# Kernel optimization log

Measured on AMD Instinct MI355X. Metric: run time of the kernel, lower is better.

## Reference

```python
import jax, jax.numpy as jnp
import numpy as np

B, S, E, D, A = 32, 2048, 1024, 1024, 1024


def setup_inputs() -> dict:
    key = jax.random.key(0)
    k1, k2, k3, k4, k5, k6, k7, k8 = jax.random.split(key, 8)
    # Kaiming-uniform-ish init scales (values don't matter for correctness)
    def lin(kw, kb, fan_in, fan_out):
        bound = 1.0 / np.sqrt(fan_in)
        W = jax.random.uniform(kw, (fan_out, fan_in), minval=-bound, maxval=bound, dtype=jnp.float32)
        b = jax.random.uniform(kb, (fan_out,), minval=-bound, maxval=bound, dtype=jnp.float32)
        return W, b
    W_enc, b_enc = lin(k1, k2, E, A)
    W_dec, b_dec = lin(k3, k4, D, A)
    W_v, b_v = lin(k5, k6, A, 1)
    encoder_out = jax.random.normal(k7, (B, S, E), dtype=jnp.float32)
    decoder_hidden = jax.random.normal(k8, (B, D), dtype=jnp.float32)
    return {
        "encoder_out": encoder_out,
        "decoder_hidden": decoder_hidden,
        "W_enc": W_enc, "b_enc": b_enc,
        "W_dec": W_dec, "b_dec": b_dec,
        "W_v": W_v, "b_v": b_v,
    }


def reference(encoder_out, decoder_hidden, W_enc, b_enc, W_dec, b_dec, W_v, b_v):
    # encoder_proj: [B, S, A]
    encoder_proj = jnp.einsum('bse,ae->bsa', encoder_out, W_enc) + b_enc
    # decoder_proj: [B, 1, A]
    decoder_proj = (jnp.einsum('bd,ad->ba', decoder_hidden, W_dec) + b_dec)[:, None, :]
    # scores: [B, S] (V projects attention_dim -> 1)
    scores = jnp.einsum('bsa,a->bs', jnp.tanh(encoder_proj + decoder_proj), W_v[0]) + b_v[0]
    alpha = jax.nn.softmax(scores, axis=1)  # [B, S]
    context = jnp.einsum('bse,bs->be', encoder_out, alpha)  # [B, E]
    return (context, alpha)
```

## Files before the change

kernel.cpp:

```cpp
#include <hip/hip_runtime.h>

typedef unsigned short ushort_t;
typedef __attribute__((ext_vector_type(8))) short short8;
typedef __attribute__((ext_vector_type(4))) float f32x4;


__device__ __forceinline__ ushort_t f2bf(float f) {
    unsigned u = __builtin_bit_cast(unsigned, f);
    u += 0x7fffu + ((u >> 16) & 1u);
    return (ushort_t)(u >> 16);
}

__device__ __forceinline__ float bf2f(ushort_t h) {
    unsigned u = ((unsigned)h) << 16;
    return __builtin_bit_cast(float, u);
}

__device__ __forceinline__ float tanh_fast(float x) {
    float e = __expf(2.0f * x);
    float r = __builtin_amdgcn_rcpf(e + 1.0f);
    return __builtin_fmaf(-2.0f, r, 1.0f);
}

__device__ __forceinline__ void gld16(const ushort_t* g, ushort_t* lds) {
    __builtin_amdgcn_global_load_lds(
        (const __attribute__((address_space(1))) unsigned int*)g,
        (__attribute__((address_space(3))) unsigned int*)lds, 16, 0, 0);
}


__global__ __launch_bounds__(256) void k_front(const float* __restrict__ enc,
                                               const float* __restrict__ Wenc,
                                               const float* __restrict__ dh,
                                               const float* __restrict__ Wd,
                                               const float* __restrict__ bd,
                                               const float* __restrict__ be,
                                               ushort_t* __restrict__ encB,
                                               ushort_t* __restrict__ wencB,
                                               float* __restrict__ dproj,
                                               float4* __restrict__ scores4) {
    const int bx = blockIdx.x;
    const int t = threadIdx.x;
    if (bx < 8192) {
        int i = bx * 256 + t;
        for (; i < 17055744; i += 2097152) {
            if (i < 16777216) {
                float4 v = ((const float4*)enc)[i];
                ushort4 o;
                o.x = f2bf(v.x); o.y = f2bf(v.y); o.z = f2bf(v.z); o.w = f2bf(v.w);
                ((ushort4*)encB)[i] = o;
            } else if (i < 17039360) {
                int j = i - 16777216;
                float4 v = ((const float4*)Wenc)[j];
                ushort4 o;
                o.x = f2bf(v.x); o.y = f2bf(v.y); o.z = f2bf(v.z); o.w = f2bf(v.w);
                ((ushort4*)wencB)[j] = o;
            } else {
                scores4[i - 17039360] = (float4){0.f, 0.f, 0.f, 0.f};
            }
        }
    } else {
        int wid = (bx - 8192) * 4 + (t >> 6);
        int lane = t & 63;
        int a = wid & 1023, b = wid >> 10;
        const float4* x = (const float4*)(dh + (size_t)b * 1024);
        const float4* wrow = (const float4*)(Wd + (size_t)a * 1024);
        float s = 0.f;
#pragma unroll
        for (int it = 0; it < 4; ++it) {
            int c = it * 64 + lane;
            float4 xv = x[c], wv = wrow[c];
            s += xv.x * wv.x + xv.y * wv.y + xv.z * wv.z + xv.w * wv.w;
        }
#pragma unroll
        for (int o = 1; o < 64; o <<= 1) s += __shfl_xor(s, o, 64);
        if (lane == 0) dproj[b * 1024 + a] = s + bd[a] + be[a];
    }
}


__global__ __launch_bounds__(256, 2) void k_gemm_scores(const ushort_t* __restrict__ A,
                                                        const ushort_t* __restrict__ Bm,
                                                        const float* __restrict__ dproj,
                                                        const float* __restrict__ Wv,
                                                        float* __restrict__ scores) {
    __shared__ __align__(16) ushort_t At[256 * 64];
    __shared__ __align__(16) ushort_t Bt[128 * 64];

    const int tid = threadIdx.x;
    const int lane = tid & 63;
    const int w = tid >> 6;
    const int wm = w >> 1, wn = w & 1;

    const int blk = blockIdx.x;
    const int q2 = blk >> 3;
    const int blkN = q2 & 7;
    const int blkM = (blk & 7) + ((q2 >> 3) << 3);
    const long long arow0 = (long long)blkM * 256;
    const int brow0 = blkN * 128;

    const int sr = lane >> 3;
    const int sgrp = lane & 7;
    const int c8s = sgrp ^ sr;

    const int q = lane >> 4;
    const int ml = lane & 15;

    const ushort_t* ga = A + (arow0 + w * 64 + sr) * 1024 + c8s * 8;
    const ushort_t* gb = Bm + (long long)(brow0 + w * 32 + sr) * 1024 + c8s * 8;

    f32x4 acc[8][4];
#pragma unroll
    for (int i = 0; i < 8; ++i)
#pragma unroll
        for (int jj = 0; jj < 4; ++jj) acc[i][jj] = (f32x4){0.f, 0.f, 0.f, 0.f};

    for (int k0 = 0; k0 < 1024; k0 += 64) {
        __syncthreads();
#pragma unroll
        for (int j = 0; j < 8; ++j)
            gld16(ga + j * 8192, &At[(w * 8 + j) * 512]);
#pragma unroll
        for (int j = 0; j < 4; ++j)
            gld16(gb + j * 8192, &Bt[(w * 4 + j) * 512]);
        ga += 64; gb += 64;
        __builtin_amdgcn_s_waitcnt(0);
        __syncthreads();

#pragma unroll
        for (int kk = 0; kk < 2; ++kk) {
            const int kb = kk * 4;
            const int slot = (kb + q) ^ (ml & 7);
            short8 af[8], bfr[4];
#pragma unroll
            for (int i = 0; i < 8; ++i) {
                int row = wm * 128 + i * 16 + ml;
                af[i] = *(const short8*)&At[row * 64 + slot * 8];
            }
#pragma unroll
            for (int jj = 0; jj < 4; ++jj) {
                int col = wn * 64 + jj * 16 + ml;
                bfr[jj] = *(const short8*)&Bt[col * 64 + slot * 8];
            }
#pragma unroll
            for (int i = 0; i < 8; ++i)
#pragma unroll
                for (int jj = 0; jj < 4; ++jj)
                    acc[i][jj] = __builtin_amdgcn_mfma_f32_16x16x32_bf16(
                        af[i], bfr[jj], acc[i][jj], 0, 0, 0);
        }
    }

    const int bb = blkM >> 3;
    float dp[4], wv[4];
#pragma unroll
    for (int jj = 0; jj < 4; ++jj) {
        int a = blkN * 128 + wn * 64 + jj * 16 + ml;
        dp[jj] = dproj[bb * 1024 + a];
        wv[jj] = Wv[a];
    }
#pragma unroll
    for (int i = 0; i < 8; ++i) {
        float rs[4] = {0.f, 0.f, 0.f, 0.f};
#pragma unroll
        for (int jj = 0; jj < 4; ++jj) {
            f32x4 v = acc[i][jj];
            rs[0] += wv[jj] * tanh_fast(v.x + dp[jj]);
            rs[1] += wv[jj] * tanh_fast(v.y + dp[jj]);
            rs[2] += wv[jj] * tanh_fast(v.z + dp[jj]);
            rs[3] += wv[jj] * tanh_fast(v.w + dp[jj]);
        }
#pragma unroll
        for (int r = 0; r < 4; ++r)
#pragma unroll
            for (int o = 1; o < 16; o <<= 1) rs[r] += __shfl_xor(rs[r], o, 64);
        if (ml == 0) {
            long long m0 = arow0 + wm * 128 + i * 16 + q * 4;
            atomicAdd(&scores[m0 + 0], rs[0]);
            atomicAdd(&scores[m0 + 1], rs[1]);
            atomicAdd(&scores[m0 + 2], rs[2]);
            atomicAdd(&scores[m0 + 3], rs[3]);
        }
    }
}


__global__ __launch_bounds__(512) void k_ctx(const ushort_t* __restrict__ encB,
                                             const float* __restrict__ scores,
                                             float* __restrict__ out) {
    const int b = blockIdx.x, ec = blockIdx.y;
    const int t = threadIdx.x;
    const int l = t & 31, g = t >> 5;
    const int lane = t & 63, wv = t >> 6;
    __shared__ float al[2048];
    __shared__ float red[8];
    __shared__ f32x4 part[16][33];

    float4 v = ((const float4*)scores)[b * 512 + t];
    float mx = fmaxf(fmaxf(v.x, v.y), fmaxf(v.z, v.w));
#pragma unroll
    for (int o = 1; o < 64; o <<= 1) mx = fmaxf(mx, __shfl_xor(mx, o, 64));
    if (lane == 0) red[wv] = mx;
    __syncthreads();
    mx = red[0];
#pragma unroll
    for (int j = 1; j < 8; ++j) mx = fmaxf(mx, red[j]);
    float e0 = __expf(v.x - mx), e1 = __expf(v.y - mx);
    float e2 = __expf(v.z - mx), e3 = __expf(v.w - mx);
    float s = e0 + e1 + e2 + e3;
#pragma unroll
    for (int o = 1; o < 64; o <<= 1) s += __shfl_xor(s, o, 64);
    __syncthreads();
    if (lane == 0) red[wv] = s;
    __syncthreads();
    s = 0.f;
#pragma unroll
    for (int j = 0; j < 8; ++j) s += red[j];
    float inv = 1.0f / s;
    float4 a4 = (float4){e0 * inv, e1 * inv, e2 * inv, e3 * inv};
    ((float4*)al)[t] = a4;
    if (ec == 0) ((float4*)(out + 32768 + (size_t)b * 2048))[t] = a4;
    __syncthreads();

    const ushort_t* ep = encB + ((size_t)b * 2048 + g) * 1024 + ec * 128 + l * 4;
    f32x4 acc = (f32x4){0.f, 0.f, 0.f, 0.f};
#pragma unroll 8
    for (int it = 0; it < 128; ++it) {
        ushort4 ev = *(const ushort4*)(ep + (size_t)it * 16384);
        float a = al[g + it * 16];
        acc.x += a * bf2f(ev.x);
        acc.y += a * bf2f(ev.y);
        acc.z += a * bf2f(ev.z);
        acc.w += a * bf2f(ev.w);
    }
    part[g][l] = acc;
    __syncthreads();
    if (t < 32) {
        f32x4 ss = part[0][t];
#pragma unroll
        for (int gg = 1; gg < 16; ++gg) {
            f32x4 pp = part[gg][t];
            ss.x += pp.x; ss.y += pp.y; ss.z += pp.z; ss.w += pp.w;
        }
        *(float4*)(out + (size_t)b * 1024 + ec * 128 + t * 4) =
            (float4){ss.x, ss.y, ss.z, ss.w};
    }
}


extern "C" void kernel_launch(void* const* d_in, const int* in_sizes, int n_in,
                              void* d_out, int out_size, void* d_ws, size_t ws_size,
                              hipStream_t stream) {
    const float* enc  = (const float*)d_in[0];
    const float* dh   = (const float*)d_in[1];
    const float* Wenc = (const float*)d_in[2];
    const float* benc = (const float*)d_in[3];
    const float* Wdec = (const float*)d_in[4];
    const float* bdec = (const float*)d_in[5];
    const float* Wv   = (const float*)d_in[6];
    float* out = (float*)d_out;

    char* ws = (char*)d_ws;
    ushort_t* encB  = (ushort_t*)ws;
    ushort_t* wencB = (ushort_t*)(ws + 134217728ull);
    float* dproj    = (float*)(ws + 134217728ull + 2097152ull);
    float* scores   = (float*)(ws + 134217728ull + 2097152ull + 131072ull);

    k_front<<<16384, 256, 0, stream>>>(enc, Wenc, dh, Wdec, bdec, benc,
                                       encB, wencB, dproj, (float4*)scores);
    k_gemm_scores<<<2048, 256, 0, stream>>>(encB, wencB, dproj, Wv, scores);
    k_ctx<<<dim3(32, 8), 512, 0, stream>>>(encB, scores, out);
}
```

Baseline: 545.9 us.

## Double-buffer LDS in scores GEMM with 256x256 tiles and 8 waves

Reworks the fused GEMM+tanh+score kernel to use 512-thread blocks computing 256x256 output tiles, halving the grid. A two-stage LDS ping-pong now issues the global-to-LDS loads for the next K-slice before the MFMAs on the current one, so load latency overlaps with compute instead of being waited on each iteration. MFMA sections are wrapped in s_setprio to favour math waves. The cost is 128KB of LDS per block, which allows only one block per CU and reduces latency hiding across blocks, despite the launch-bounds hint of two.

```diff
diff --git a/kernel.cpp b/kernel.cpp
--- a/kernel.cpp
+++ b/kernel.cpp
@@ -79,25 +79,26 @@
 }
 
 
-__global__ __launch_bounds__(256, 2) void k_gemm_scores(const ushort_t* __restrict__ A,
+__global__ __launch_bounds__(512, 2) void k_gemm_scores(const ushort_t* __restrict__ A,
                                                         const ushort_t* __restrict__ Bm,
                                                         const float* __restrict__ dproj,
                                                         const float* __restrict__ Wv,
                                                         float* __restrict__ scores) {
-    __shared__ __align__(16) ushort_t At[256 * 64];
-    __shared__ __align__(16) ushort_t Bt[128 * 64];
+    __shared__ __align__(16) ushort_t At[2][256 * 64];
+    __shared__ __align__(16) ushort_t Bt[2][256 * 64];
 
     const int tid = threadIdx.x;
     const int lane = tid & 63;
     const int w = tid >> 6;
-    const int wm = w >> 1, wn = w & 1;
+    const int wm = w >> 2, wn = w & 3;
 
     const int blk = blockIdx.x;
-    const int q2 = blk >> 3;
-    const int blkN = q2 & 7;
-    const int blkM = (blk & 7) + ((q2 >> 3) << 3);
+    const int xcd = blk & 7;
+    const int idx = blk >> 3;
+    const int blkN = idx & 3;
+    const int blkM = xcd + ((idx >> 2) << 3);
     const long long arow0 = (long long)blkM * 256;
-    const int brow0 = blkN * 128;
+    const int brow0 = blkN * 256;
 
     const int sr = lane >> 3;
     const int sgrp = lane & 7;
@@ -106,8 +107,8 @@
     const int q = lane >> 4;
     const int ml = lane & 15;
 
-    const ushort_t* ga = A + (arow0 + w * 64 + sr) * 1024 + c8s * 8;
-    const ushort_t* gb = Bm + (long long)(brow0 + w * 32 + sr) * 1024 + c8s * 8;
+    const ushort_t* ga = A + (arow0 + w * 8 + sr) * 1024 + c8s * 8;
+    const ushort_t* gb = Bm + (long long)(brow0 + w * 8 + sr) * 1024 + c8s * 8;
 
     f32x4 acc[8][4];
 #pragma unroll
@@ -115,18 +116,24 @@
 #pragma unroll
         for (int jj = 0; jj < 4; ++jj) acc[i][jj] = (f32x4){0.f, 0.f, 0.f, 0.f};
 
-    for (int k0 = 0; k0 < 1024; k0 += 64) {
-        __syncthreads();
-#pragma unroll
-        for (int j = 0; j < 8; ++j)
-            gld16(ga + j * 8192, &At[(w * 8 + j) * 512]);
-#pragma unroll
-        for (int j = 0; j < 4; ++j)
-            gld16(gb + j * 8192, &Bt[(w * 4 + j) * 512]);
-        ga += 64; gb += 64;
-        __builtin_amdgcn_s_waitcnt(0);
-        __syncthreads();
-
+#pragma unroll
+    for (int j = 0; j < 4; ++j) gld16(ga + j * 65536, &At[0][w * 512 + j * 4096]);
+#pragma unroll
+    for (int j = 0; j < 4; ++j) gld16(gb + j * 65536, &Bt[0][w * 512 + j * 4096]);
+    ga += 64; gb += 64;
+    __builtin_amdgcn_s_waitcnt(0);
+    __syncthreads();
+
+    for (int t = 0; t < 16; ++t) {
+        const int cur = t & 1;
+        if (t < 15) {
+            const int nxt = cur ^ 1;
+#pragma unroll
+            for (int j = 0; j < 4; ++j) gld16(ga + j * 65536, &At[nxt][w * 512 + j * 4096]);
+#pragma unroll
+            for (int j = 0; j < 4; ++j) gld16(gb + j * 65536, &Bt[nxt][w * 512 + j * 4096]);
+            ga += 64; gb += 64;
+        }
 #pragma unroll
         for (int kk = 0; kk < 2; ++kk) {
             const int kb = kk * 4;
@@ -135,27 +142,31 @@
 #pragma unroll
             for (int i = 0; i < 8; ++i) {
                 int row = wm * 128 + i * 16 + ml;
-                af[i] = *(const short8*)&At[row * 64 + slot * 8];
+                af[i] = *(const short8*)&At[cur][row * 64 + slot * 8];
             }
 #pragma unroll
             for (int jj = 0; jj < 4; ++jj) {
                 int col = wn * 64 + jj * 16 + ml;
-                bfr[jj] = *(const short8*)&Bt[col * 64 + slot * 8];
+                bfr[jj] = *(const short8*)&Bt[cur][col * 64 + slot * 8];
             }
+            __builtin_amdgcn_s_setprio(1);
 #pragma unroll
             for (int i = 0; i < 8; ++i)
 #pragma unroll
                 for (int jj = 0; jj < 4; ++jj)
                     acc[i][jj] = __builtin_amdgcn_mfma_f32_16x16x32_bf16(
                         af[i], bfr[jj], acc[i][jj], 0, 0, 0);
-        }
+            __builtin_amdgcn_s_setprio(0);
+        }
+        __builtin_amdgcn_s_waitcnt(0);
+        __syncthreads();
     }
 
     const int bb = blkM >> 3;
     float dp[4], wv[4];
 #pragma unroll
     for (int jj = 0; jj < 4; ++jj) {
-        int a = blkN * 128 + wn * 64 + jj * 16 + ml;
+        int a = blkN * 256 + wn * 64 + jj * 16 + ml;
         dp[jj] = dproj[bb * 1024 + a];
         wv[jj] = Wv[a];
     }
@@ -268,6 +279,6 @@
 
     k_front<<<16384, 256, 0, stream>>>(enc, Wenc, dh, Wdec, bdec, benc,
                                        encB, wencB, dproj, (float4*)scores);
-    k_gemm_scores<<<2048, 256, 0, stream>>>(encB, wencB, dproj, Wv, scores);
+    k_gemm_scores<<<1024, 512, 0, stream>>>(encB, wencB, dproj, Wv, scores);
     k_ctx<<<dim3(32, 8), 512, 0, stream>>>(encB, scores, out);
 }
```

New measurement: 574.1 us. 5.2% more time.
